# Kernel optimization log

Measured on AMD Instinct MI355X. Metric: run time of the kernel, lower is better.

The kernel has to match this reference:

```python
import jax, jax.numpy as jnp
import numpy as np

H, KV, D, HID, Q, S = 16, 8, 128, 2048, 1024, 8192
CACHE_POS = 4096

def rotate_half(x, axis):
    x1, x2 = jnp.split(x, 2, axis)
    return jnp.concatenate((-x2, x1), axis=axis)

def setup_inputs() -> dict:
    key = jax.random.key(0)
    ks = jax.random.split(key, 12)
    hidden_states = jax.random.normal(ks[0], (1, HID, 1, Q), jnp.float32)
    # RoPE tables for the new token positions [CACHE_POS, CACHE_POS+Q)
    pos = jnp.arange(CACHE_POS, CACHE_POS + Q, dtype=jnp.float32)
    inv_freq = 1.0 / (10000.0 ** (jnp.arange(0, D, 2, dtype=jnp.float32) / D))
    ang = pos[:, None] * inv_freq[None, :]                      # (Q, D/2)
    cos = jnp.tile(jnp.cos(ang), (1, 2))[None, None]            # (1,1,Q,D)
    sin = jnp.tile(jnp.sin(ang), (1, 2))[None, None]
    cos_t = jnp.transpose(cos, (0, 1, 3, 2))                    # (1,1,D,Q)
    sin_t = jnp.transpose(sin, (0, 1, 3, 2))
    # causal mask over full cache: key slot s visible to query i iff s <= CACHE_POS + i
    k_idx = jnp.arange(S)[:, None]
    q_idx = jnp.arange(Q)[None, :]
    attention_mask = jnp.where(k_idx <= CACHE_POS + q_idx, 0.0, -1e9).astype(jnp.float32)[None, None]  # (1,1,S,Q)
    key_cache = 0.02 * jax.random.normal(ks[1], (1, KV, S, D), jnp.float32)
    value_cache = 0.02 * jax.random.normal(ks[2], (1, KV, S, D), jnp.float32)
    w = lambda k, shp: 0.02 * jax.random.normal(k, shp, jnp.float32)
    return dict(hidden_states=hidden_states, cos=cos, sin=sin, cos_t=cos_t, sin_t=sin_t,
                attention_mask=attention_mask, key_cache=key_cache, value_cache=value_cache,
                Wq=w(ks[3], (HID, HID)), bq=w(ks[4], (HID,)),
                Wk=w(ks[5], (KV * D, HID)), bk=w(ks[6], (KV * D,)),
                Wv=w(ks[7], (KV * D, HID)), bv=w(ks[8], (KV * D,)),
                Wo=w(ks[9], (HID, HID)), cache_position=CACHE_POS)

def reference(hidden_states, cos, sin, cos_t, sin_t, attention_mask,
              key_cache, value_cache, Wq, bq, Wk, bk, Wv, bv, Wo, cache_position):
    # 1x1-conv style projections on channels-first (1, C, 1, Q)
    q = jnp.einsum('oc,bcxq->boxq', Wq, hidden_states) + bq[None, :, None, None]
    k = jnp.einsum('oc,bcxq->boxq', Wk, hidden_states) + bk[None, :, None, None]
    v = jnp.einsum('oc,bcxq->boxq', Wv, hidden_states) + bv[None, :, None, None]
    q = q.reshape(1, H, D, Q)                                   # (1,H,D,Q)
    k = k.reshape(1, KV, D, Q).transpose(0, 1, 3, 2)            # (1,KV,Q,D)
    v = v.reshape(1, KV, D, Q).transpose(0, 1, 3, 2)
    # inline RoPE: q along head_dim axis (-2), k along last axis
    q = q * cos_t + rotate_half(q, -2) * sin_t
    k = k * cos + rotate_half(k, -1) * sin
    # KV-cache scatter at layer_idx=0, offset cache_position
    key_cache = jax.lax.dynamic_update_slice(key_cache, k, (0, 0, cache_position, 0))
    value_cache = jax.lax.dynamic_update_slice(value_cache, v, (0, 0, cache_position, 0))
    k_all = key_cache[0]                                        # (KV,S,D)
    v_all = value_cache[0]
    qg = q.reshape(KV, H // KV, D, Q)                           # GQA groups
    scores = jnp.einsum('ksd,kgdq->kgsq', k_all, qg) / jnp.sqrt(jnp.float32(D))
    scores = scores + attention_mask[0]                         # (1,S,Q) broadcast
    w = jax.nn.softmax(scores, axis=2)                          # softmax over cache slots
    out = jnp.einsum('kgsq,ksd->kgdq', w, v_all)                # (KV,G,D,Q)
    out = out.reshape(1, H * D, 1, Q)
    attn_output = jnp.einsum('oc,bcxq->boxq', Wo, out)
    return attn_output
```

## Files before the change

### kernel.cpp

```cpp
#include <hip/hip_runtime.h>

#define H_HEADS 16
#define KV_HEADS 8
#define DHEAD 128
#define HID 2048
#define NQ 1024
#define SCACHE 8192
#define CPOS 4096
#define SEFF 5120

typedef __attribute__((ext_vector_type(8))) __bf16 bf16x8;
typedef __attribute__((ext_vector_type(4))) float f32x4;
typedef unsigned short u16;
typedef unsigned int u32;

__device__ __forceinline__ u16 f2b(float f) {
  u32 u = __float_as_uint(f);
  u += 0x7fffu + ((u >> 16) & 1u);
  return (u16)(u >> 16);
}
__device__ __forceinline__ u16 f2b_t(float f) {
  return (u16)(__float_as_uint(f) >> 16);
}
__device__ __forceinline__ float b2f(u16 b) { return __uint_as_float(((u32)b) << 16); }
__device__ __forceinline__ u32 pk2(u16 a, u16 b) { return (u32)a | ((u32)b << 16); }
__device__ __forceinline__ uint2 f4b4(float4 v) {
  uint2 o;
  o.x = pk2(f2b(v.x), f2b(v.y));
  o.y = pk2(f2b(v.z), f2b(v.w));
  return o;
}

union U4 { uint4 v; u16 u[8]; };

__global__ void __launch_bounds__(256) k_conv_w(const float* __restrict__ Wq,
                                                const float* __restrict__ Wk,
                                                const float* __restrict__ Wv,
                                                u16* __restrict__ Wb) {
  int i = blockIdx.x * 256 + threadIdx.x;
  const float* src;
  int off;
  if (i < 1048576) { src = Wq; off = i; }
  else if (i < 1572864) { src = Wk; off = i - 1048576; }
  else { src = Wv; off = i - 1572864; }
  float4 v = ((const float4*)src)[off];
  *(uint2*)(Wb + (size_t)i * 4) = f4b4(v);
}

__global__ void __launch_bounds__(256) k_f32_to_bf16(const float* __restrict__ src,
                                                     u16* __restrict__ dst, int n4) {
  int i = blockIdx.x * 256 + threadIdx.x;
  if (i < n4) {
    float4 v = ((const float4*)src)[i];
    *(uint2*)(dst + (size_t)i * 4) = f4b4(v);
  }
}

__global__ void __launch_bounds__(256) k_transpose_h(const float* __restrict__ hid,
                                                     u16* __restrict__ hT) {
  __shared__ __align__(16) float ls[64 * 68];
  int t = threadIdx.x;
  int c0 = blockIdx.x * 64, q0 = blockIdx.y * 64;
#pragma unroll
  for (int it = 0; it < 4; ++it) {
    int c = it * 256 + t;
    int row = c >> 4, ch = c & 15;
    *(float4*)(ls + row * 68 + ch * 4) =
        *(const float4*)(hid + (size_t)(c0 + row) * NQ + q0 + ch * 4);
  }
  __syncthreads();
  int ql = t & 63, cch = t >> 6;
  u32 ob[8];
#pragma unroll
  for (int j = 0; j < 8; ++j)
    ob[j] = pk2(f2b(ls[(cch * 16 + 2 * j) * 68 + ql]), f2b(ls[(cch * 16 + 2 * j + 1) * 68 + ql]));
  uint4* dst = (uint4*)(hT + (size_t)(q0 + ql) * HID + c0 + cch * 16);
  dst[0] = make_uint4(ob[0], ob[1], ob[2], ob[3]);
  dst[1] = make_uint4(ob[4], ob[5], ob[6], ob[7]);
}

__global__ void __launch_bounds__(256) k_prep_vT(const float* __restrict__ vc,
                                                 u16* __restrict__ vT) {
  __shared__ __align__(16) float ls[64 * 132];
  int t = threadIdx.x;
  int s0 = blockIdx.x * 64;
  int kv = blockIdx.y;
#pragma unroll
  for (int it = 0; it < 8; ++it) {
    int c = it * 256 + t;
    int row = c >> 5, ch = c & 31;
    *(float4*)(ls + row * 132 + ch * 4) =
        *(const float4*)(vc + ((size_t)kv * SCACHE + s0 + row) * DHEAD + ch * 4);
  }
  __syncthreads();
  int d = t >> 1, sch = t & 1;
  u32 ob[16];
#pragma unroll
  for (int j = 0; j < 16; ++j)
    ob[j] = pk2(f2b(ls[(sch * 32 + 2 * j) * 132 + d]), f2b(ls[(sch * 32 + 2 * j + 1) * 132 + d]));
  uint4* dst = (uint4*)(vT + ((size_t)kv * DHEAD + d) * SEFF + s0 + sch * 32);
#pragma unroll
  for (int j = 0; j < 4; ++j)
    dst[j] = make_uint4(ob[4 * j], ob[4 * j + 1], ob[4 * j + 2], ob[4 * j + 3]);
}

__global__ void __launch_bounds__(256) k_conv_k(const float* __restrict__ kc,
                                                u16* __restrict__ kb) {
  int i = blockIdx.x * 256 + threadIdx.x;
  int kvi = i >> 17;
  int rem = i & 131071;
  float4 v = *(const float4*)(kc + (size_t)kvi * SCACHE * DHEAD + (size_t)rem * 4);
  *(uint2*)(kb + (size_t)kvi * SEFF * DHEAD + (size_t)rem * 4) = f4b4(v);
}

__global__ void __launch_bounds__(256) k_copy_vnew(const u16* __restrict__ qkv,
                                                   u16* __restrict__ vT) {
  int i = blockIdx.x * 256 + threadIdx.x;
  int row = i >> 7, ch = i & 127;
  *(uint4*)(vT + (size_t)row * SEFF + CPOS + ch * 8) =
      *(const uint4*)(qkv + (size_t)(3072 + row) * NQ + ch * 8);
}

__global__ void __launch_bounds__(256) k_rope_t(const u16* __restrict__ qkv,
                                                const float* __restrict__ cosb,
                                                const float* __restrict__ sinb,
                                                u16* __restrict__ qb,
                                                u16* __restrict__ kb) {
  __shared__ __align__(16) u16 ls[64 * 136];
  int t = threadIdx.x;
  int hh = blockIdx.x;
  int q0 = blockIdx.y * 64;
  bool isq = hh < 16;
  int rowbase = isq ? hh * DHEAD : HID + (hh - 16) * DHEAD;
#pragma unroll
  for (int it = 0; it < 4; ++it) {
    int c = it * 256 + t;
    int d = c >> 3, qc = (c & 7) * 8;
    U4 v;
    v.v = *(const uint4*)(qkv + (size_t)(rowbase + d) * NQ + q0 + qc);
#pragma unroll
    for (int e = 0; e < 8; ++e) ls[(qc + e) * 136 + d] = v.u[e];
  }
  __syncthreads();
  int ql = t & 63, hf = t >> 6;
  int q = q0 + ql;
  float scale = isq ? 0.08838834764831845f : 1.0f;
  u16* dst = isq ? (qb + ((size_t)hh * NQ + q) * DHEAD)
                 : (kb + ((size_t)(hh - 16) * SEFF + CPOS + q) * DHEAD);
#pragma unroll
  for (int g = 0; g < 4; ++g) {
    int d0 = hf * 32 + g * 8;
    U4 x, y;
    x.v = *(uint4*)(ls + ql * 136 + d0);
    y.v = *(uint4*)(ls + ql * 136 + (d0 ^ 64));
    float4 ca = *(const float4*)(cosb + (size_t)q * DHEAD + d0);
    float4 cb = *(const float4*)(cosb + (size_t)q * DHEAD + d0 + 4);
    float4 sa = *(const float4*)(sinb + (size_t)q * DHEAD + d0);
    float4 sb = *(const float4*)(sinb + (size_t)q * DHEAD + d0 + 4);
    float cs[8] = {ca.x, ca.y, ca.z, ca.w, cb.x, cb.y, cb.z, cb.w};
    float sn[8] = {sa.x, sa.y, sa.z, sa.w, sb.x, sb.y, sb.z, sb.w};
    float sgn = (d0 < 64) ? -1.0f : 1.0f;
    u32 ob[4];
#pragma unroll
    for (int e = 0; e < 4; ++e) {
      float r0 = (b2f(x.u[2 * e]) * cs[2 * e] + sgn * b2f(y.u[2 * e]) * sn[2 * e]) * scale;
      float r1 = (b2f(x.u[2 * e + 1]) * cs[2 * e + 1] + sgn * b2f(y.u[2 * e + 1]) * sn[2 * e + 1]) * scale;
      ob[e] = pk2(f2b(r0), f2b(r1));
    }
    *(uint4*)(dst + d0) = make_uint4(ob[0], ob[1], ob[2], ob[3]);
  }
}

__global__ void __launch_bounds__(256) k_gemm_qkv(
    const u16* __restrict__ Wb, const u16* __restrict__ hT, u16* __restrict__ qkv,
    const float* __restrict__ bq, const float* __restrict__ bk, const float* __restrict__ bv) {
  __shared__ __align__(16) u16 lsA[128 * 32];
  __shared__ __align__(16) u16 lsB[128 * 32];
  int t = threadIdx.x;
  int m0 = blockIdx.x * 128, n0 = blockIdx.y * 128;
  const u16* Abase = Wb + (size_t)m0 * HID;
  int lane = t & 63, wid = t >> 6;
  int quad = lane >> 4, l15 = lane & 15;
  int wr = wid >> 1, wc = wid & 1;
  f32x4 acc[4][4];
#pragma unroll
  for (int i = 0; i < 4; ++i)
#pragma unroll
    for (int j = 0; j < 4; ++j) acc[i][j] = (f32x4){0.f, 0.f, 0.f, 0.f};
  for (int kt = 0; kt < HID; kt += 32) {
    __syncthreads();
#pragma unroll
    for (int it = 0; it < 2; ++it) {
      int c = it * 256 + t;
      int row = c >> 2, ch = c & 3;
      *(uint4*)(lsA + row * 32 + ch * 8) =
          *(const uint4*)(Abase + (size_t)row * HID + kt + ch * 8);
      *(uint4*)(lsB + row * 32 + ch * 8) =
          *(const uint4*)(hT + (size_t)(n0 + row) * HID + kt + ch * 8);
    }
    __syncthreads();
    bf16x8 af[4], bfr[4];
#pragma unroll
    for (int i = 0; i < 4; ++i)
      af[i] = *(const bf16x8*)(lsA + (wr * 64 + i * 16 + l15) * 32 + quad * 8);
#pragma unroll
    for (int j = 0; j < 4; ++j)
      bfr[j] = *(const bf16x8*)(lsB + (wc * 64 + j * 16 + l15) * 32 + quad * 8);
#pragma unroll
    for (int i = 0; i < 4; ++i)
#pragma unroll
      for (int j = 0; j < 4; ++j)
        acc[i][j] = __builtin_amdgcn_mfma_f32_16x16x32_bf16(af[i], bfr[j], acc[i][j], 0, 0, 0);
  }
#pragma unroll
  for (int i = 0; i < 4; ++i) {
#pragma unroll
    for (int r = 0; r < 4; ++r) {
      int m = m0 + wr * 64 + i * 16 + quad * 4 + r;
      float bias = (m < 2048) ? bq[m] : ((m < 3072) ? bk[m - 2048] : bv[m - 3072]);
#pragma unroll
      for (int j = 0; j < 4; ++j) {
        int n = n0 + wc * 64 + j * 16 + l15;
        qkv[(size_t)m * NQ + n] = f2b(acc[i][j][r] + bias);
      }
    }
  }
}

__global__ void __launch_bounds__(512) k_flash(const u16* __restrict__ qb,
                                               const u16* __restrict__ kb,
                                               const u16* __restrict__ vT,
                                               u16* __restrict__ po,
                                               float* __restrict__ pm,
                                               float* __restrict__ pl) {
  __shared__ __align__(16) u16 lsK[64 * 136];
  __shared__ __align__(16) u16 lsV[128 * 72];
  __shared__ __align__(16) u16 lsP[8 * 16 * 72];
  int t = threadIdx.x;
  int h = blockIdx.x, qt = blockIdx.y, z = blockIdx.z;
  int kv = h >> 1;
  int q0 = qt * 128;
  int lane = t & 63, wid = t >> 6;
  int quad = lane >> 4, l15 = lane & 15;
  int qw = q0 + wid * 16;

  union { u16 u[8]; bf16x8 v; } onesu;
#pragma unroll
  for (int e = 0; e < 8; ++e) onesu.u[e] = 0x3f80;
  bf16x8 onesf = onesu.v;

  bf16x8 qf[4];
  const u16* qrow = qb + ((size_t)h * NQ + qw + l15) * DHEAD;
#pragma unroll
  for (int kc = 0; kc < 4; ++kc) qf[kc] = *(const bf16x8*)(qrow + kc * 32 + quad * 8);
  f32x4 oacc[8];
#pragma unroll
  for (int f = 0; f < 8; ++f) oacc[f] = (f32x4){0.f, 0.f, 0.f, 0.f};
  f32x4 lacc = (f32x4){0.f, 0.f, 0.f, 0.f};
  float m_run[4];
#pragma unroll
  for (int r = 0; r < 4; ++r) m_run[r] = -1e30f;
  u16* lsPw = lsP + wid * (16 * 72);
  int Svis = CPOS + q0 + 128;
  const u16* kbase = kb + (size_t)kv * SEFF * DHEAD;
  const u16* vbase = vT + (size_t)kv * DHEAD * SEFF;

  int rK = t >> 4, cK = (t & 15) * 8;
  int rV = t >> 3, cV = (t & 7) * 8;
  uint4 pk0, pk1, pv0, pv1;
  {
    int s0 = z * 64;
    pk0 = *(const uint4*)(kbase + (size_t)(s0 + rK) * DHEAD + cK);
    pk1 = *(const uint4*)(kbase + (size_t)(s0 + 32 + rK) * DHEAD + cK);
    pv0 = *(const uint4*)(vbase + (size_t)rV * SEFF + s0 + cV);
    pv1 = *(const uint4*)(vbase + (size_t)(64 + rV) * SEFF + s0 + cV);
  }
  for (int s0 = z * 64; s0 < Svis; s0 += 256) {
    __syncthreads();
    *(uint4*)(lsK + rK * 136 + cK) = pk0;
    *(uint4*)(lsK + (32 + rK) * 136 + cK) = pk1;
    *(uint4*)(lsV + rV * 72 + cV) = pv0;
    *(uint4*)(lsV + (64 + rV) * 72 + cV) = pv1;
    __syncthreads();
    int sn = s0 + 256;
    if (sn < Svis) {
      pk0 = *(const uint4*)(kbase + (size_t)(sn + rK) * DHEAD + cK);
      pk1 = *(const uint4*)(kbase + (size_t)(sn + 32 + rK) * DHEAD + cK);
      pv0 = *(const uint4*)(vbase + (size_t)rV * SEFF + sn + cV);
      pv1 = *(const uint4*)(vbase + (size_t)(64 + rV) * SEFF + sn + cV);
    }
    f32x4 sc[4];
#pragma unroll
    for (int js = 0; js < 4; ++js) {
      sc[js] = (f32x4){0.f, 0.f, 0.f, 0.f};
#pragma unroll
      for (int kc = 0; kc < 4; ++kc) {
        bf16x8 kf = *(const bf16x8*)(lsK + (js * 16 + l15) * 136 + kc * 32 + quad * 8);
        sc[js] = __builtin_amdgcn_mfma_f32_16x16x32_bf16(qf[kc], kf, sc[js], 0, 0, 0);
      }
    }
    if (s0 + 63 > CPOS + qw) {
#pragma unroll
      for (int r = 0; r < 4; ++r) {
        int lim = CPOS + qw + quad * 4 + r - s0;
#pragma unroll
        for (int js = 0; js < 4; ++js) {
          bool valid = (js * 16 + l15) <= lim;
          sc[js][r] = valid ? sc[js][r] : -1e30f;
        }
      }
    }
    float alpha[4];
#pragma unroll
    for (int r = 0; r < 4; ++r) {
      float mx = fmaxf(fmaxf(sc[0][r], sc[1][r]), fmaxf(sc[2][r], sc[3][r]));
      mx = fmaxf(mx, __shfl_xor(mx, 1, 64));
      mx = fmaxf(mx, __shfl_xor(mx, 2, 64));
      mx = fmaxf(mx, __shfl_xor(mx, 4, 64));
      mx = fmaxf(mx, __shfl_xor(mx, 8, 64));
      float mnew = fmaxf(m_run[r], mx);
      alpha[r] = __expf(m_run[r] - mnew);
      m_run[r] = mnew;
#pragma unroll
      for (int js = 0; js < 4; ++js) {
        float p = __expf(sc[js][r] - mnew);
        lsPw[(quad * 4 + r) * 72 + js * 16 + l15] = f2b_t(p);
      }
    }
#pragma unroll
    for (int f = 0; f < 8; ++f)
#pragma unroll
      for (int r = 0; r < 4; ++r) oacc[f][r] *= alpha[r];
#pragma unroll
    for (int r = 0; r < 4; ++r) lacc[r] *= alpha[r];
    bf16x8 pf[2];
#pragma unroll
    for (int ks = 0; ks < 2; ++ks)
      pf[ks] = *(const bf16x8*)(lsPw + l15 * 72 + ks * 32 + quad * 8);
#pragma unroll
    for (int f = 0; f < 8; ++f) {
#pragma unroll
      for (int ks = 0; ks < 2; ++ks) {
        bf16x8 vf = *(const bf16x8*)(lsV + (f * 16 + l15) * 72 + ks * 32 + quad * 8);
        oacc[f] = __builtin_amdgcn_mfma_f32_16x16x32_bf16(pf[ks], vf, oacc[f], 0, 0, 0);
      }
    }
#pragma unroll
    for (int ks = 0; ks < 2; ++ks)
      lacc = __builtin_amdgcn_mfma_f32_16x16x32_bf16(pf[ks], onesf, lacc, 0, 0, 0);
  }
  int p = (h * 8 + qt) * 4 + z;
#pragma unroll
  for (int r = 0; r < 4; ++r) {
    int qloc = wid * 16 + quad * 4 + r;
    if (l15 == 0) {
      pm[(size_t)p * 128 + qloc] = m_run[r];
      pl[(size_t)p * 128 + qloc] = lacc[r];
    }
#pragma unroll
    for (int f = 0; f < 8; ++f)
      po[(size_t)p * 16384 + qloc * 128 + f * 16 + l15] = f2b(oacc[f][r]);
  }
}

__global__ void __launch_bounds__(256) k_combine(const u16* __restrict__ po,
                                                 const float* __restrict__ pm,
                                                 const float* __restrict__ pl,
                                                 u16* __restrict__ outT) {
  int t = threadIdx.x;
  int h = blockIdx.x, qt = blockIdx.y;
  int q = qt * 64 + (t >> 2);
  int dq = (t & 3) * 32;
  int pb = (h * 8 + (q >> 7)) * 4;
  int ql = q & 127;
  float m0 = pm[(size_t)(pb + 0) * 128 + ql];
  float m1 = pm[(size_t)(pb + 1) * 128 + ql];
  float m2 = pm[(size_t)(pb + 2) * 128 + ql];
  float m3 = pm[(size_t)(pb + 3) * 128 + ql];
  float M = fmaxf(fmaxf(m0, m1), fmaxf(m2, m3));
  float w[4] = {__expf(m0 - M), __expf(m1 - M), __expf(m2 - M), __expf(m3 - M)};
  float L = 0.f;
#pragma unroll
  for (int zz = 0; zz < 4; ++zz) L += w[zz] * pl[(size_t)(pb + zz) * 128 + ql];
  float acc[32];
#pragma unroll
  for (int e = 0; e < 32; ++e) acc[e] = 0.f;
#pragma unroll
  for (int zz = 0; zz < 4; ++zz) {
    const u16* src = po + (size_t)(pb + zz) * 16384 + ql * 128 + dq;
#pragma unroll
    for (int j = 0; j < 4; ++j) {
      U4 v;
      v.v = *(const uint4*)(src + j * 8);
#pragma unroll
      for (int e = 0; e < 8; ++e) acc[j * 8 + e] += w[zz] * b2f(v.u[e]);
    }
  }
  float inv = 1.0f / L;
  u16* dst = outT + (size_t)q * HID + h * DHEAD + dq;
#pragma unroll
  for (int j = 0; j < 4; ++j) {
    u32 ob[4];
#pragma unroll
    for (int e = 0; e < 4; ++e)
      ob[e] = pk2(f2b(acc[j * 8 + 2 * e] * inv), f2b(acc[j * 8 + 2 * e + 1] * inv));
    *(uint4*)(dst + j * 8) = make_uint4(ob[0], ob[1], ob[2], ob[3]);
  }
}

__global__ void __launch_bounds__(256) k_gemm_bt(const u16* __restrict__ A,
                                                 const u16* __restrict__ BT,
                                                 float* __restrict__ C) {
  __shared__ __align__(16) u16 lsA[128 * 32];
  __shared__ __align__(16) u16 lsB[64 * 32];
  int t = threadIdx.x;
  int m0 = blockIdx.x * 128, n0 = blockIdx.y * 64;
  const u16* Abase = A + (size_t)m0 * HID;
  const u16* Bbase = BT + (size_t)n0 * HID;
  int lane = t & 63, wid = t >> 6;
  int quad = lane >> 4, l15 = lane & 15;
  int wr = wid >> 1, wc = wid & 1;
  f32x4 acc[4][2];
#pragma unroll
  for (int i = 0; i < 4; ++i)
#pragma unroll
    for (int j = 0; j < 2; ++j) acc[i][j] = (f32x4){0.f, 0.f, 0.f, 0.f};
  for (int kt = 0; kt < HID; kt += 32) {
    __syncthreads();
#pragma unroll
    for (int it = 0; it < 2; ++it) {
      int c = it * 256 + t;
      int row = c >> 2, ch = c & 3;
      *(uint4*)(lsA + row * 32 + ch * 8) =
          *(const uint4*)(Abase + (size_t)row * HID + kt + ch * 8);
    }
    {
      int row = t >> 2, ch = t & 3;
      *(uint4*)(lsB + row * 32 + ch * 8) =
          *(const uint4*)(Bbase + (size_t)row * HID + kt + ch * 8);
    }
    __syncthreads();
    bf16x8 af[4], bfr[2];
#pragma unroll
    for (int i = 0; i < 4; ++i)
      af[i] = *(const bf16x8*)(lsA + (wr * 64 + i * 16 + l15) * 32 + quad * 8);
#pragma unroll
    for (int j = 0; j < 2; ++j)
      bfr[j] = *(const bf16x8*)(lsB + (wc * 32 + j * 16 + l15) * 32 + quad * 8);
#pragma unroll
    for (int i = 0; i < 4; ++i)
#pragma unroll
      for (int j = 0; j < 2; ++j)
        acc[i][j] = __builtin_amdgcn_mfma_f32_16x16x32_bf16(af[i], bfr[j], acc[i][j], 0, 0, 0);
  }
#pragma unroll
  for (int i = 0; i < 4; ++i)
#pragma unroll
    for (int r = 0; r < 4; ++r) {
      int m = m0 + wr * 64 + i * 16 + quad * 4 + r;
#pragma unroll
      for (int j = 0; j < 2; ++j) {
        int n = n0 + wc * 32 + j * 16 + l15;
        C[(size_t)m * NQ + n] = acc[i][j][r];
      }
    }
}

extern "C" void kernel_launch(void* const* d_in, const int* in_sizes, int n_in,
                              void* d_out, int out_size, void* d_ws, size_t ws_size,
                              hipStream_t stream) {
  (void)in_sizes; (void)n_in; (void)out_size; (void)ws_size;
  const float* hidden = (const float*)d_in[0];
  const float* cosb = (const float*)d_in[1];
  const float* sinb = (const float*)d_in[2];
  const float* kcache = (const float*)d_in[6];
  const float* vcache = (const float*)d_in[7];
  const float* Wq = (const float*)d_in[8];
  const float* bq = (const float*)d_in[9];
  const float* Wk = (const float*)d_in[10];
  const float* bk = (const float*)d_in[11];
  const float* Wv = (const float*)d_in[12];
  const float* bv = (const float*)d_in[13];
  const float* Wo = (const float*)d_in[14];

  char* ws = (char*)d_ws;
  u16* qkv = (u16*)(ws);
  u16* outT = (u16*)(ws + 8388608);
  u16* hT = outT;
  u16* vT = (u16*)(ws + 12582912);
  u16* Wob = vT;
  u16* kb = (u16*)(ws + 23068672);
  u16* qb = (u16*)(ws + 33554432);
  u16* Wb = (u16*)(ws + 12582912);
  u16* po = (u16*)(ws + 37748736);
  float* pm = (float*)(ws + 54525952);
  float* pl = (float*)(ws + 54788096);
  float* outb = (float*)d_out;

  k_conv_w<<<8192, 256, 0, stream>>>(Wq, Wk, Wv, Wb);
  k_transpose_h<<<dim3(32, 16), 256, 0, stream>>>(hidden, hT);
  k_gemm_qkv<<<dim3(32, 8), 256, 0, stream>>>(Wb, hT, qkv, bq, bk, bv);
  k_prep_vT<<<dim3(64, 8), 256, 0, stream>>>(vcache, vT);
  k_conv_k<<<4096, 256, 0, stream>>>(kcache, kb);
  k_rope_t<<<dim3(24, 16), 256, 0, stream>>>(qkv, cosb, sinb, qb, kb);
  k_copy_vnew<<<512, 256, 0, stream>>>(qkv, vT);
  k_flash<<<dim3(16, 8, 4), 512, 0, stream>>>(qb, kb, vT, po, pm, pl);
  k_f32_to_bf16<<<4096, 256, 0, stream>>>(Wo, Wob, 1048576);
  k_combine<<<dim3(16, 16), 256, 0, stream>>>(po, pm, pl, outT);
  k_gemm_bt<<<dim3(16, 16), 256, 0, stream>>>(Wob, outT, outb);
}
```

Before: 365.4 us.

## Use direct global-to-LDS loads in GEMMs and XOR-swizzle flash-attention LDS

The two projection GEMMs now stage tiles with global_load_lds (16-byte direct-to-LDS loads) instead of going through registers. The flash kernel replaces padded LDS rows for K, V and P with an XOR swizzle, cutting LDS footprint while avoiding bank conflicts. It also skips the output-accumulator rescale when no lane's running max changed. Risks: correct ordering of the direct-to-LDS loads relies on the existing barriers plus compiler-inserted waits, and global_load_lds with 16-byte width needs hardware that supports it.

```diff
diff --git a/kernel.cpp b/kernel.cpp
--- a/kernel.cpp
+++ b/kernel.cpp
@@ -29,6 +29,11 @@
   o.x = pk2(f2b(v.x), f2b(v.y));
   o.y = pk2(f2b(v.z), f2b(v.w));
   return o;
+}
+
+__device__ __forceinline__ void gld16(const u16* g, u16* l) {
+  __builtin_amdgcn_global_load_lds((const __attribute__((address_space(1))) void*)g,
+                                   (__attribute__((address_space(3))) void*)l, 16, 0, 0);
 }
 
 union U4 { uint4 v; u16 u[8]; };
@@ -193,10 +198,8 @@
     for (int it = 0; it < 2; ++it) {
       int c = it * 256 + t;
       int row = c >> 2, ch = c & 3;
-      *(uint4*)(lsA + row * 32 + ch * 8) =
-          *(const uint4*)(Abase + (size_t)row * HID + kt + ch * 8);
-      *(uint4*)(lsB + row * 32 + ch * 8) =
-          *(const uint4*)(hT + (size_t)(n0 + row) * HID + kt + ch * 8);
+      gld16(Abase + (size_t)row * HID + kt + ch * 8, lsA + row * 32 + ch * 8);
+      gld16(hT + (size_t)(n0 + row) * HID + kt + ch * 8, lsB + row * 32 + ch * 8);
     }
     __syncthreads();
     bf16x8 af[4], bfr[4];
@@ -233,9 +236,9 @@
                                                u16* __restrict__ po,
                                                float* __restrict__ pm,
                                                float* __restrict__ pl) {
-  __shared__ __align__(16) u16 lsK[64 * 136];
-  __shared__ __align__(16) u16 lsV[128 * 72];
-  __shared__ __align__(16) u16 lsP[8 * 16 * 72];
+  __shared__ __align__(16) u16 lsK[64 * 128];
+  __shared__ __align__(16) u16 lsV[128 * 64];
+  __shared__ __align__(16) u16 lsP[8 * 16 * 64];
   int t = threadIdx.x;
   int h = blockIdx.x, qt = blockIdx.y, z = blockIdx.z;
   int kv = h >> 1;
@@ -243,6 +246,7 @@
   int lane = t & 63, wid = t >> 6;
   int quad = lane >> 4, l15 = lane & 15;
   int qw = q0 + wid * 16;
+  int xr = (l15 & 7) << 3;
 
   union { u16 u[8]; bf16x8 v; } onesu;
 #pragma unroll
@@ -260,13 +264,15 @@
   float m_run[4];
 #pragma unroll
   for (int r = 0; r < 4; ++r) m_run[r] = -1e30f;
-  u16* lsPw = lsP + wid * (16 * 72);
+  u16* lsPw = lsP + wid * (16 * 64);
   int Svis = CPOS + q0 + 128;
   const u16* kbase = kb + (size_t)kv * SEFF * DHEAD;
   const u16* vbase = vT + (size_t)kv * DHEAD * SEFF;
 
   int rK = t >> 4, cK = (t & 15) * 8;
   int rV = t >> 3, cV = (t & 7) * 8;
+  int xwK = (rK & 7) << 3;
+  int xwV = (rV & 7) << 3;
   uint4 pk0, pk1, pv0, pv1;
   {
     int s0 = z * 64;
@@ -277,10 +283,10 @@
   }
   for (int s0 = z * 64; s0 < Svis; s0 += 256) {
     __syncthreads();
-    *(uint4*)(lsK + rK * 136 + cK) = pk0;
-    *(uint4*)(lsK + (32 + rK) * 136 + cK) = pk1;
-    *(uint4*)(lsV + rV * 72 + cV) = pv0;
-    *(uint4*)(lsV + (64 + rV) * 72 + cV) = pv1;
+    *(uint4*)(lsK + rK * 128 + (cK ^ xwK)) = pk0;
+    *(uint4*)(lsK + (32 + rK) * 128 + (cK ^ xwK)) = pk1;
+    *(uint4*)(lsV + rV * 64 + (cV ^ xwV)) = pv0;
+    *(uint4*)(lsV + (64 + rV) * 64 + (cV ^ xwV)) = pv1;
     __syncthreads();
     int sn = s0 + 256;
     if (sn < Svis) {
@@ -295,7 +301,7 @@
       sc[js] = (f32x4){0.f, 0.f, 0.f, 0.f};
 #pragma unroll
       for (int kc = 0; kc < 4; ++kc) {
-        bf16x8 kf = *(const bf16x8*)(lsK + (js * 16 + l15) * 136 + kc * 32 + quad * 8);
+        bf16x8 kf = *(const bf16x8*)(lsK + (js * 16 + l15) * 128 + ((kc * 32 + quad * 8) ^ xr));
         sc[js] = __builtin_amdgcn_mfma_f32_16x16x32_bf16(qf[kc], kf, sc[js], 0, 0, 0);
       }
     }
@@ -321,27 +327,32 @@
       float mnew = fmaxf(m_run[r], mx);
       alpha[r] = __expf(m_run[r] - mnew);
       m_run[r] = mnew;
+      int prow = quad * 4 + r;
+      int pxw = (prow & 7) << 3;
 #pragma unroll
       for (int js = 0; js < 4; ++js) {
         float p = __expf(sc[js][r] - mnew);
-        lsPw[(quad * 4 + r) * 72 + js * 16 + l15] = f2b_t(p);
+        lsPw[prow * 64 + ((js * 16 + l15) ^ pxw)] = f2b_t(p);
       }
     }
-#pragma unroll
-    for (int f = 0; f < 8; ++f)
-#pragma unroll
-      for (int r = 0; r < 4; ++r) oacc[f][r] *= alpha[r];
-#pragma unroll
-    for (int r = 0; r < 4; ++r) lacc[r] *= alpha[r];
+    bool needresc = (alpha[0] < 1.f) | (alpha[1] < 1.f) | (alpha[2] < 1.f) | (alpha[3] < 1.f);
+    if (__any(needresc)) {
+#pragma unroll
+      for (int f = 0; f < 8; ++f)
+#pragma unroll
+        for (int r = 0; r < 4; ++r) oacc[f][r] *= alpha[r];
+#pragma unroll
+      for (int r = 0; r < 4; ++r) lacc[r] *= alpha[r];
+    }
     bf16x8 pf[2];
 #pragma unroll
     for (int ks = 0; ks < 2; ++ks)
-      pf[ks] = *(const bf16x8*)(lsPw + l15 * 72 + ks * 32 + quad * 8);
+      pf[ks] = *(const bf16x8*)(lsPw + l15 * 64 + ((ks * 32 + quad * 8) ^ xr));
 #pragma unroll
     for (int f = 0; f < 8; ++f) {
 #pragma unroll
       for (int ks = 0; ks < 2; ++ks) {
-        bf16x8 vf = *(const bf16x8*)(lsV + (f * 16 + l15) * 72 + ks * 32 + quad * 8);
+        bf16x8 vf = *(const bf16x8*)(lsV + (f * 16 + l15) * 64 + ((ks * 32 + quad * 8) ^ xr));
         oacc[f] = __builtin_amdgcn_mfma_f32_16x16x32_bf16(pf[ks], vf, oacc[f], 0, 0, 0);
       }
     }
@@ -431,13 +442,11 @@
     for (int it = 0; it < 2; ++it) {
       int c = it * 256 + t;
       int row = c >> 2, ch = c & 3;
-      *(uint4*)(lsA + row * 32 + ch * 8) =
-          *(const uint4*)(Abase + (size_t)row * HID + kt + ch * 8);
+      gld16(Abase + (size_t)row * HID + kt + ch * 8, lsA + row * 32 + ch * 8);
     }
     {
       int row = t >> 2, ch = t & 3;
-      *(uint4*)(lsB + row * 32 + ch * 8) =
-          *(const uint4*)(Bbase + (size_t)row * HID + kt + ch * 8);
+      gld16(Bbase + (size_t)row * HID + kt + ch * 8, lsB + row * 32 + ch * 8);
     }
     __syncthreads();
     bf16x8 af[4], bfr[2];
```

Result: no change. 371.7 us (+1.7%).
